# Optimization experiments

Hardware: AMD Instinct MI355X
Metric: run time of the kernel (lower is better)

The kernel has to match this reference:

```python
import jax, jax.numpy as jnp
import numpy as np

N_NODES = 100000
N_EDGES = 1600000
IN_CH, HID_CH, OUT_CH = 256, 128, 64


def setup_inputs() -> dict:
    key = jax.random.key(0)
    k_x, k_e, k1, k2, kb1, kb2 = jax.random.split(key, 6)
    x = jax.random.normal(k_x, (N_NODES, IN_CH), dtype=jnp.float32)
    edge_index = jax.random.randint(k_e, (2, N_EDGES), 0, N_NODES, dtype=jnp.int64)
    # Glorot-style init for GCN linear weights
    W1 = jax.random.normal(k1, (IN_CH, HID_CH), dtype=jnp.float32) * (1.0 / np.sqrt(IN_CH))
    b1 = jnp.zeros((HID_CH,), dtype=jnp.float32)
    W2 = jax.random.normal(k2, (HID_CH, OUT_CH), dtype=jnp.float32) * (1.0 / np.sqrt(HID_CH))
    b2 = jnp.zeros((OUT_CH,), dtype=jnp.float32)
    return {"x": x, "edge_index": edge_index, "W1": W1, "b1": b1, "W2": W2, "b2": b2}


def _gcn_norm(edge_index, n_nodes):
    # add self loops, compute D^{-1/2} (A+I) D^{-1/2} edge weights (PyG gcn_norm)
    loop = jnp.arange(n_nodes, dtype=edge_index.dtype)
    src = jnp.concatenate([edge_index[0], loop])
    dst = jnp.concatenate([edge_index[1], loop])
    deg = jax.ops.segment_sum(jnp.ones_like(src, dtype=jnp.float32), dst, num_segments=n_nodes)
    dinv = jnp.where(deg > 0, jax.lax.rsqrt(jnp.maximum(deg, 1.0)), 0.0)
    norm = dinv[src] * dinv[dst]  # [E + N]
    return src, dst, norm


def _gcn_conv(x, W, b, src, dst, norm, n_nodes):
    h = x @ W                         # linear first (PyG GCNConv)
    msg = norm[:, None] * h[src]      # gather + normalize  [E+N, out]
    agg = jax.ops.segment_sum(msg, dst, num_segments=n_nodes)
    return agg + b


def reference(x, edge_index, W1, b1, W2, b2):
    n = x.shape[0]
    src, dst, norm = _gcn_norm(edge_index, n)
    h = jax.nn.relu(_gcn_conv(x, W1, b1, src, dst, norm, n))
    # dropout is identity in eval mode
    z = _gcn_conv(h, W2, b2, src, dst, norm, n)
    # inner-product decoder on the provided edges, with sigmoid
    e_src, e_dst = edge_index[0], edge_index[1]
    logits = jnp.sum(z[e_src] * z[e_dst], axis=-1)
    return jax.nn.sigmoid(logits)
```

## Files before the change

kernel.cpp:

```cpp
#include <hip/hip_runtime.h>
#include <math.h>

#define N_NODES 100000
#define N_EDGES 1600000
#define IN_CH 256
#define HID_CH 128
#define OUT_CH 64
#define NTILES ((N_NODES + 63) / 64)
#define NB 1024
#define NPART 256
#define EPB (N_EDGES / NPART)
#define NB_USED ((N_NODES + 127) / 128)

typedef short s16x8 __attribute__((ext_vector_type(8)));
typedef unsigned short u16x8 __attribute__((ext_vector_type(8)));
typedef float f32x4 __attribute__((ext_vector_type(4)));

__device__ __forceinline__ float bf2f(unsigned short u) {
    union { unsigned int i; float f; } v;
    v.i = ((unsigned int)u) << 16;
    return v.f;
}
__device__ __forceinline__ unsigned short f2bf(float f) {
    union { float f; unsigned int i; } v;
    v.f = f;
    unsigned int u = v.i;
    return (unsigned short)((u + 0x7FFFu + ((u >> 16) & 1u)) >> 16);
}


__global__ __launch_bounds__(256) void k_hist(const int* __restrict__ dst,
                                              int* __restrict__ ghist) {
    __shared__ int h[NB];
    int b = blockIdx.x, t = threadIdx.x;
    for (int k = t; k < NB; k += 256) h[k] = 0;
    __syncthreads();
    int e0 = b * EPB;
    for (int e = e0 + t; e < e0 + EPB; e += 256)
        atomicAdd(&h[dst[e] >> 7], 1);
    __syncthreads();
    for (int k = t; k < NB; k += 256) ghist[k * NPART + b] = h[k];
}

__global__ __launch_bounds__(256) void k_scan_cols(const int* __restrict__ ghist,
                                                   int* __restrict__ goff,
                                                   int* __restrict__ btot) {
    __shared__ int tmp[NPART];
    int k = blockIdx.x, t = threadIdx.x;
    int v = ghist[k * NPART + t];
    tmp[t] = v;
    __syncthreads();
    for (int off = 1; off < NPART; off <<= 1) {
        int u = (t >= off) ? tmp[t - off] : 0;
        __syncthreads();
        tmp[t] += u;
        __syncthreads();
    }
    goff[k * NPART + t] = tmp[t] - v;
    if (t == NPART - 1) btot[k] = tmp[t];
}

__global__ __launch_bounds__(1024) void k_scan_base(const int* __restrict__ btot,
                                                    int* __restrict__ bbase) {
    __shared__ int tmp[NB];
    int t = threadIdx.x;
    int v = btot[t];
    tmp[t] = v;
    __syncthreads();
    for (int off = 1; off < NB; off <<= 1) {
        int u = (t >= off) ? tmp[t - off] : 0;
        __syncthreads();
        tmp[t] += u;
        __syncthreads();
    }
    bbase[t] = tmp[t] - v;
    if (t == NB - 1) bbase[NB] = tmp[t];
}

__global__ __launch_bounds__(256) void k_partition(const int* __restrict__ src,
                                                   const int* __restrict__ dst,
                                                   const int* __restrict__ goff,
                                                   const int* __restrict__ bbase,
                                                   int2* __restrict__ bsorted) {
    __shared__ int cur[NB];
    int b = blockIdx.x, t = threadIdx.x;
    for (int k = t; k < NB; k += 256) cur[k] = bbase[k] + goff[k * NPART + b];
    __syncthreads();
    int e0 = b * EPB;
    for (int e = e0 + t; e < e0 + EPB; e += 256) {
        int s = src[e], d = dst[e];
        int pos = atomicAdd(&cur[d >> 7], 1);
        bsorted[pos] = make_int2(s, d);
    }
}

__global__ __launch_bounds__(256) void k_bucket_csr(const int2* __restrict__ bsorted,
                                                    const int* __restrict__ bbase,
                                                    int* __restrict__ rowoff,
                                                    float* __restrict__ dinv,
                                                    int* __restrict__ csr_src) {
    __shared__ int cnt[128];
    __shared__ int tmp[256];
    __shared__ int cur[128];
    int b = blockIdx.x, t = threadIdx.x;
    int ebeg = bbase[b], eend = bbase[b + 1];
    if (t < 128) cnt[t] = 0;
    __syncthreads();
    for (int e = ebeg + t; e < eend; e += 256)
        atomicAdd(&cnt[bsorted[e].y & 127], 1);
    __syncthreads();
    int v = (t < 128) ? cnt[t] : 0;
    tmp[t] = v;
    __syncthreads();
    for (int off = 1; off < 256; off <<= 1) {
        int u = (t >= off) ? tmp[t - off] : 0;
        __syncthreads();
        tmp[t] += u;
        __syncthreads();
    }
    if (t < 128) {
        int base = ebeg + tmp[t] - v;
        cur[t] = base;
        int node = b * 128 + t;
        if (node < N_NODES) {
            rowoff[node] = base;
            dinv[node] = rsqrtf((float)v + 1.0f);
        }
    }
    __syncthreads();
    for (int e = ebeg + t; e < eend; e += 256) {
        int2 ed = bsorted[e];
        int pos = atomicAdd(&cur[ed.y & 127], 1);
        csr_src[pos] = ed.x;
    }
}

__global__ __launch_bounds__(256) void k_cast(const float* __restrict__ x,
                                              unsigned short* __restrict__ xb) {
    const int total = N_NODES * IN_CH / 8;
    int stride = gridDim.x * 256;
    for (int i = blockIdx.x * 256 + threadIdx.x; i < total; i += stride) {
        f32x4 a = *reinterpret_cast<const f32x4*>(x + (size_t)i * 8);
        f32x4 b = *reinterpret_cast<const f32x4*>(x + (size_t)i * 8 + 4);
        u16x8 o;
        o[0] = f2bf(a[0]); o[1] = f2bf(a[1]); o[2] = f2bf(a[2]); o[3] = f2bf(a[3]);
        o[4] = f2bf(b[0]); o[5] = f2bf(b[1]); o[6] = f2bf(b[2]); o[7] = f2bf(b[3]);
        *reinterpret_cast<u16x8*>(xb + (size_t)i * 8) = o;
    }
}

__global__ void k_wt1(const float* __restrict__ W1, unsigned short* __restrict__ Wf1) {
    int u = blockIdx.x * 256 + threadIdx.x;
    int f = u >> 6, lane = u & 63;
    int kk = f >> 3, nt = f & 7;
    int l15 = lane & 15, lhi = lane >> 4;
    int n = nt * 16 + l15;
    int kbase = kk * 32 + lhi * 8;
    #pragma unroll
    for (int j = 0; j < 8; ++j)
        Wf1[(size_t)u * 8 + j] = f2bf(W1[(size_t)(kbase + j) * HID_CH + n]);
}

__global__ void k_wt2(const float* __restrict__ W2, unsigned short* __restrict__ Wf2) {
    int u = blockIdx.x * 256 + threadIdx.x;
    int f = u >> 6, lane = u & 63;
    int kk = f >> 2, nt = f & 3;
    int l15 = lane & 15, lhi = lane >> 4;
    int n = nt * 16 + l15;
    int kbase = kk * 32 + lhi * 8;
    #pragma unroll
    for (int j = 0; j < 8; ++j)
        Wf2[(size_t)u * 8 + j] = f2bf(W2[(size_t)(kbase + j) * OUT_CH + n]);
}

__global__ __launch_bounds__(256, 4) void k_gemm1(const unsigned short* __restrict__ xb,
                                                  const unsigned short* __restrict__ Wf1,
                                                  const float* __restrict__ dinv,
                                                  unsigned short* __restrict__ hs1) {
    int tid = threadIdx.x;
    int w = tid >> 6;
    int lane = tid & 63;
    int l15 = lane & 15;
    int lhi = lane >> 4;
    int m0 = blockIdx.x * 64;

    int arow = m0 + w * 16 + l15;
    int arowc = (arow < N_NODES) ? arow : (N_NODES - 1);
    const s16x8* ap = reinterpret_cast<const s16x8*>(xb + (size_t)arowc * IN_CH) + lhi;

    s16x8 af[8];
    #pragma unroll
    for (int kk = 0; kk < 8; ++kk) af[kk] = ap[kk * 4];

    const s16x8* wp = reinterpret_cast<const s16x8*>(Wf1) + lane;

    f32x4 acc[8] = {};
    #pragma unroll
    for (int kk = 0; kk < 8; ++kk) {
        #pragma unroll
        for (int nt = 0; nt < 8; ++nt) {
            s16x8 bf = wp[(kk * 8 + nt) * 64];
            acc[nt] = __builtin_amdgcn_mfma_f32_16x16x32_bf16(af[kk], bf, acc[nt], 0, 0, 0);
        }
    }

    float dv[4];
    int rb = m0 + w * 16 + lhi * 4;
    #pragma unroll
    for (int r = 0; r < 4; ++r) dv[r] = (rb + r < N_NODES) ? dinv[rb + r] : 0.0f;
    #pragma unroll
    for (int nt = 0; nt < 8; ++nt) {
        #pragma unroll
        for (int r = 0; r < 4; ++r) {
            int row = rb + r;
            if (row < N_NODES)
                hs1[(size_t)row * HID_CH + nt * 16 + l15] = f2bf(dv[r] * acc[nt][r]);
        }
    }
}

__global__ __launch_bounds__(256, 4) void k_gemm2(const unsigned short* __restrict__ h1r,
                                                  const unsigned short* __restrict__ Wf2,
                                                  const float* __restrict__ dinv,
                                                  unsigned short* __restrict__ hs2) {
    int tid = threadIdx.x;
    int w = tid >> 6;
    int lane = tid & 63;
    int l15 = lane & 15;
    int lhi = lane >> 4;
    int m0 = blockIdx.x * 64;

    int arow = m0 + w * 16 + l15;
    int arowc = (arow < N_NODES) ? arow : (N_NODES - 1);
    const s16x8* ap = reinterpret_cast<const s16x8*>(h1r + (size_t)arowc * HID_CH) + lhi;

    s16x8 af[4];
    #pragma unroll
    for (int kk = 0; kk < 4; ++kk) af[kk] = ap[kk * 4];

    const s16x8* wp = reinterpret_cast<const s16x8*>(Wf2) + lane;

    f32x4 acc[4] = {};
    #pragma unroll
    for (int kk = 0; kk < 4; ++kk) {
        #pragma unroll
        for (int nt = 0; nt < 4; ++nt) {
            s16x8 bf = wp[(kk * 4 + nt) * 64];
            acc[nt] = __builtin_amdgcn_mfma_f32_16x16x32_bf16(af[kk], bf, acc[nt], 0, 0, 0);
        }
    }

    float dv[4];
    int rb = m0 + w * 16 + lhi * 4;
    #pragma unroll
    for (int r = 0; r < 4; ++r) dv[r] = (rb + r < N_NODES) ? dinv[rb + r] : 0.0f;
    #pragma unroll
    for (int nt = 0; nt < 4; ++nt) {
        #pragma unroll
        for (int r = 0; r < 4; ++r) {
            int row = rb + r;
            if (row < N_NODES)
                hs2[(size_t)row * OUT_CH + nt * 16 + l15] = f2bf(dv[r] * acc[nt][r]);
        }
    }
}

template <int C, bool RELU>
__global__ __launch_bounds__(256) void k_gather_agg(const int* __restrict__ rowoff,
                                                    const int* __restrict__ csr_src,
                                                    const unsigned short* __restrict__ hs,
                                                    const float* __restrict__ dinv,
                                                    const float* __restrict__ b,
                                                    unsigned short* __restrict__ outp) {
    constexpr int TPN = C / 8;
    constexpr int NPB = 256 / TPN;
    int t = threadIdx.x;
    int node = blockIdx.x * NPB + t / TPN;
    int q = t % TPN;
    if (node >= N_NODES) return;

    int beg = rowoff[node];
    int end = (node + 1 < N_NODES) ? rowoff[node + 1] : N_EDGES;

    float acc[8];
    {
        u16x8 sv = *reinterpret_cast<const u16x8*>(&hs[(size_t)node * C + q * 8]);
        #pragma unroll
        for (int j = 0; j < 8; ++j) acc[j] = bf2f(sv[j]);
    }

    int i = beg;
    for (; i + 1 < end; i += 2) {
        int s0 = csr_src[i];
        int s1 = csr_src[i + 1];
        u16x8 v0 = *reinterpret_cast<const u16x8*>(&hs[(size_t)s0 * C + q * 8]);
        u16x8 v1 = *reinterpret_cast<const u16x8*>(&hs[(size_t)s1 * C + q * 8]);
        #pragma unroll
        for (int j = 0; j < 8; ++j) acc[j] += bf2f(v0[j]) + bf2f(v1[j]);
    }
    if (i < end) {
        int s0 = csr_src[i];
        u16x8 v0 = *reinterpret_cast<const u16x8*>(&hs[(size_t)s0 * C + q * 8]);
        #pragma unroll
        for (int j = 0; j < 8; ++j) acc[j] += bf2f(v0[j]);
    }

    float w = dinv[node];
    float4 b0 = reinterpret_cast<const float4*>(b)[q * 2];
    float4 b1 = reinterpret_cast<const float4*>(b)[q * 2 + 1];
    float bb[8] = {b0.x, b0.y, b0.z, b0.w, b1.x, b1.y, b1.z, b1.w};
    u16x8 o;
    #pragma unroll
    for (int j = 0; j < 8; ++j) {
        float v = w * acc[j] + bb[j];
        if (RELU) v = fmaxf(v, 0.0f);
        o[j] = f2bf(v);
    }
    *reinterpret_cast<u16x8*>(&outp[(size_t)node * C + q * 8]) = o;
}


__global__ __launch_bounds__(256) void k_decode(const int* __restrict__ esrc,
                                                const int* __restrict__ edst,
                                                const unsigned short* __restrict__ z,
                                                float* __restrict__ out) {
    int tid = threadIdx.x;
    int e = blockIdx.x * 32 + tid / 8;
    int q = tid % 8;
    if (e >= N_EDGES) return;
    int s = esrc[e], d = edst[e];
    u16x8 a = *reinterpret_cast<const u16x8*>(&z[(size_t)s * OUT_CH + q * 8]);
    u16x8 b = *reinterpret_cast<const u16x8*>(&z[(size_t)d * OUT_CH + q * 8]);
    float dot = 0.0f;
    #pragma unroll
    for (int j = 0; j < 8; ++j) dot += bf2f(a[j]) * bf2f(b[j]);
    dot += __shfl_xor(dot, 1);
    dot += __shfl_xor(dot, 2);
    dot += __shfl_xor(dot, 4);
    if (q == 0) out[e] = 1.0f / (1.0f + expf(-dot));
}


extern "C" void kernel_launch(void* const* d_in, const int* in_sizes, int n_in,
                              void* d_out, int out_size, void* d_ws, size_t ws_size,
                              hipStream_t stream) {
    const float* x  = (const float*)d_in[0];
    const int*   ei = (const int*)d_in[1];
    const float* W1 = (const float*)d_in[2];
    const float* b1 = (const float*)d_in[3];
    const float* W2 = (const float*)d_in[4];
    const float* b2 = (const float*)d_in[5];
    float* out = (float*)d_out;

    const int* src = ei;
    const int* dst = ei + N_EDGES;

    char* ws = (char*)d_ws;
    int*   ghist   = (int*)(ws + 0x000000);
    int*   goff    = (int*)(ws + 0x100000);
    int*   btot    = (int*)(ws + 0x200000);
    int*   bbase   = (int*)(ws + 0x202000);
    int*   rowoff  = (int*)(ws + 0x210000);
    float* dinv    = (float*)(ws + 0x290000);
    unsigned short* Wf1 = (unsigned short*)(ws + 0x310000);
    unsigned short* Wf2 = (unsigned short*)(ws + 0x320000);
    int*   csr_src = (int*)(ws + 0x400000);
    int2*  bsorted = (int2*)(ws + 0xB00000);
    unsigned short* xb  = (unsigned short*)(ws + 0xB00000);
    unsigned short* hs1 = (unsigned short*)(ws + 0x3C00000);
    unsigned short* h1r = (unsigned short*)(ws + 0xB00000);
    unsigned short* hs2 = (unsigned short*)(ws + 0x3C00000);
    unsigned short* z   = (unsigned short*)(ws + 0x2800000);

    k_hist<<<NPART, 256, 0, stream>>>(dst, ghist);
    k_scan_cols<<<NB, 256, 0, stream>>>(ghist, goff, btot);
    k_scan_base<<<1, NB, 0, stream>>>(btot, bbase);
    k_partition<<<NPART, 256, 0, stream>>>(src, dst, goff, bbase, bsorted);
    k_bucket_csr<<<NB_USED, 256, 0, stream>>>(bsorted, bbase, rowoff, dinv, csr_src);

    k_cast<<<2048, 256, 0, stream>>>(x, xb);
    k_wt1<<<16, 256, 0, stream>>>(W1, Wf1);
    k_wt2<<<4, 256, 0, stream>>>(W2, Wf2);

    k_gemm1<<<NTILES, 256, 0, stream>>>(xb, Wf1, dinv, hs1);
    k_gather_agg<HID_CH, true><<<(N_NODES * 16 + 255) / 256, 256, 0, stream>>>(
        rowoff, csr_src, hs1, dinv, b1, h1r);

    k_gemm2<<<NTILES, 256, 0, stream>>>(h1r, Wf2, dinv, hs2);
    k_gather_agg<OUT_CH, false><<<(N_NODES * 8 + 255) / 256, 256, 0, stream>>>(
        rowoff, csr_src, hs2, dinv, b2, z);

    k_decode<<<N_EDGES / 32, 256, 0, stream>>>(src, dst, z, out);
}
```

Before: 264.3 us.

## Slice GEMM outputs into 16-column planes and gather per plane with LDS-staged indices

The GEMM epilogues now write their outputs as column-sliced planes of 16 channels (32 bytes per node), so each aggregation pass touches a small plane that fits better in cache. A 2D grid processes one plane per blockIdx.y for 128 nodes, staging the CSR source indices for those nodes in shared memory and unrolling the neighbor loop by four. In exchange, the index list is loaded once per plane and each gathered row is only 32 bytes. The GEMM stores also become more scattered.

```diff
diff --git a/kernel.cpp b/kernel.cpp
--- a/kernel.cpp
+++ b/kernel.cpp
@@ -11,6 +11,7 @@
 #define NPART 256
 #define EPB (N_EDGES / NPART)
 #define NB_USED ((N_NODES + 127) / 128)
+#define LCAP 4096
 
 typedef short s16x8 __attribute__((ext_vector_type(8)));
 typedef unsigned short u16x8 __attribute__((ext_vector_type(8)));
@@ -176,7 +177,7 @@
 __global__ __launch_bounds__(256, 4) void k_gemm1(const unsigned short* __restrict__ xb,
                                                   const unsigned short* __restrict__ Wf1,
                                                   const float* __restrict__ dinv,
-                                                  unsigned short* __restrict__ hs1) {
+                                                  unsigned short* __restrict__ hs1s) {
     int tid = threadIdx.x;
     int w = tid >> 6;
     int lane = tid & 63;
@@ -214,7 +215,7 @@
         for (int r = 0; r < 4; ++r) {
             int row = rb + r;
             if (row < N_NODES)
-                hs1[(size_t)row * HID_CH + nt * 16 + l15] = f2bf(dv[r] * acc[nt][r]);
+                hs1s[((size_t)nt * N_NODES + row) * 16 + l15] = f2bf(dv[r] * acc[nt][r]);
         }
     }
 }
@@ -222,7 +223,7 @@
 __global__ __launch_bounds__(256, 4) void k_gemm2(const unsigned short* __restrict__ h1r,
                                                   const unsigned short* __restrict__ Wf2,
                                                   const float* __restrict__ dinv,
-                                                  unsigned short* __restrict__ hs2) {
+                                                  unsigned short* __restrict__ hs2s) {
     int tid = threadIdx.x;
     int w = tid >> 6;
     int lane = tid & 63;
@@ -260,54 +261,73 @@
         for (int r = 0; r < 4; ++r) {
             int row = rb + r;
             if (row < N_NODES)
-                hs2[(size_t)row * OUT_CH + nt * 16 + l15] = f2bf(dv[r] * acc[nt][r]);
+                hs2s[((size_t)nt * N_NODES + row) * 16 + l15] = f2bf(dv[r] * acc[nt][r]);
         }
     }
 }
 
 template <int C, bool RELU>
-__global__ __launch_bounds__(256) void k_gather_agg(const int* __restrict__ rowoff,
-                                                    const int* __restrict__ csr_src,
-                                                    const unsigned short* __restrict__ hs,
-                                                    const float* __restrict__ dinv,
-                                                    const float* __restrict__ b,
-                                                    unsigned short* __restrict__ outp) {
-    constexpr int TPN = C / 8;
-    constexpr int NPB = 256 / TPN;
-    int t = threadIdx.x;
-    int node = blockIdx.x * NPB + t / TPN;
-    int q = t % TPN;
+__global__ __launch_bounds__(256) void k_gather_sl(const int* __restrict__ rowoff,
+                                                   const int* __restrict__ csr_src,
+                                                   const unsigned short* __restrict__ hsS,
+                                                   const float* __restrict__ dinv,
+                                                   const float* __restrict__ b,
+                                                   unsigned short* __restrict__ outp) {
+    __shared__ int lidx[LCAP];
+    int bx = blockIdx.x, p = blockIdx.y, t = threadIdx.x;
+    int n0 = bx * 128;
+    int ebeg = rowoff[n0];
+    int eend = (n0 + 128 < N_NODES) ? rowoff[n0 + 128] : N_EDGES;
+    int cnt = eend - ebeg;
+
+    for (int i = t; i < cnt && i < LCAP; i += 256) lidx[i] = csr_src[ebeg + i];
+    __syncthreads();
+
+    int node = n0 + (t >> 1);
+    int q = t & 1;
     if (node >= N_NODES) return;
 
-    int beg = rowoff[node];
-    int end = (node + 1 < N_NODES) ? rowoff[node + 1] : N_EDGES;
+    const unsigned short* P = hsS + (size_t)p * N_NODES * 16;
+    int lbeg = rowoff[node] - ebeg;
+    int lend = ((node + 1 < N_NODES) ? rowoff[node + 1] : N_EDGES) - ebeg;
 
     float acc[8];
     {
-        u16x8 sv = *reinterpret_cast<const u16x8*>(&hs[(size_t)node * C + q * 8]);
+        u16x8 sv = *reinterpret_cast<const u16x8*>(P + ((size_t)node << 4) + (q << 3));
         #pragma unroll
         for (int j = 0; j < 8; ++j) acc[j] = bf2f(sv[j]);
     }
 
-    int i = beg;
-    for (; i + 1 < end; i += 2) {
-        int s0 = csr_src[i];
-        int s1 = csr_src[i + 1];
-        u16x8 v0 = *reinterpret_cast<const u16x8*>(&hs[(size_t)s0 * C + q * 8]);
-        u16x8 v1 = *reinterpret_cast<const u16x8*>(&hs[(size_t)s1 * C + q * 8]);
-        #pragma unroll
-        for (int j = 0; j < 8; ++j) acc[j] += bf2f(v0[j]) + bf2f(v1[j]);
-    }
-    if (i < end) {
-        int s0 = csr_src[i];
-        u16x8 v0 = *reinterpret_cast<const u16x8*>(&hs[(size_t)s0 * C + q * 8]);
-        #pragma unroll
-        for (int j = 0; j < 8; ++j) acc[j] += bf2f(v0[j]);
+    if (cnt <= LCAP) {
+        int i = lbeg;
+        for (; i + 3 < lend; i += 4) {
+            int s0 = lidx[i], s1 = lidx[i + 1], s2 = lidx[i + 2], s3 = lidx[i + 3];
+            u16x8 v0 = *reinterpret_cast<const u16x8*>(P + ((size_t)s0 << 4) + (q << 3));
+            u16x8 v1 = *reinterpret_cast<const u16x8*>(P + ((size_t)s1 << 4) + (q << 3));
+            u16x8 v2 = *reinterpret_cast<const u16x8*>(P + ((size_t)s2 << 4) + (q << 3));
+            u16x8 v3 = *reinterpret_cast<const u16x8*>(P + ((size_t)s3 << 4) + (q << 3));
+            #pragma unroll
+            for (int j = 0; j < 8; ++j)
+                acc[j] += (bf2f(v0[j]) + bf2f(v1[j])) + (bf2f(v2[j]) + bf2f(v3[j]));
+        }
+        for (; i < lend; ++i) {
+            int s0 = lidx[i];
+            u16x8 v0 = *reinterpret_cast<const u16x8*>(P + ((size_t)s0 << 4) + (q << 3));
+            #pragma unroll
+            for (int j = 0; j < 8; ++j) acc[j] += bf2f(v0[j]);
+        }
+    } else {
+        for (int i = lbeg; i < lend; ++i) {
+            int s0 = csr_src[ebeg + i];
+            u16x8 v0 = *reinterpret_cast<const u16x8*>(P + ((size_t)s0 << 4) + (q << 3));
+            #pragma unroll
+            for (int j = 0; j < 8; ++j) acc[j] += bf2f(v0[j]);
+        }
     }
 
     float w = dinv[node];
-    float4 b0 = reinterpret_cast<const float4*>(b)[q * 2];
-    float4 b1 = reinterpret_cast<const float4*>(b)[q * 2 + 1];
+    float4 b0 = *reinterpret_cast<const float4*>(&b[p * 16 + q * 8]);
+    float4 b1 = *reinterpret_cast<const float4*>(&b[p * 16 + q * 8 + 4]);
     float bb[8] = {b0.x, b0.y, b0.z, b0.w, b1.x, b1.y, b1.z, b1.w};
     u16x8 o;
     #pragma unroll
@@ -316,7 +336,7 @@
         if (RELU) v = fmaxf(v, 0.0f);
         o[j] = f2bf(v);
     }
-    *reinterpret_cast<u16x8*>(&outp[(size_t)node * C + q * 8]) = o;
+    *reinterpret_cast<u16x8*>(outp + (size_t)node * C + p * 16 + (q << 3)) = o;
 }
 
 
@@ -366,11 +386,11 @@
     unsigned short* Wf2 = (unsigned short*)(ws + 0x320000);
     int*   csr_src = (int*)(ws + 0x400000);
     int2*  bsorted = (int2*)(ws + 0xB00000);
-    unsigned short* xb  = (unsigned short*)(ws + 0xB00000);
-    unsigned short* hs1 = (unsigned short*)(ws + 0x3C00000);
-    unsigned short* h1r = (unsigned short*)(ws + 0xB00000);
-    unsigned short* hs2 = (unsigned short*)(ws + 0x3C00000);
-    unsigned short* z   = (unsigned short*)(ws + 0x2800000);
+    unsigned short* xb   = (unsigned short*)(ws + 0xB00000);
+    unsigned short* hs1s = (unsigned short*)(ws + 0x3C00000);
+    unsigned short* h1r  = (unsigned short*)(ws + 0xB00000);
+    unsigned short* hs2s = (unsigned short*)(ws + 0x3C00000);
+    unsigned short* z    = (unsigned short*)(ws + 0x2800000);
 
     k_hist<<<NPART, 256, 0, stream>>>(dst, ghist);
     k_scan_cols<<<NB, 256, 0, stream>>>(ghist, goff, btot);
@@ -382,13 +402,13 @@
     k_wt1<<<16, 256, 0, stream>>>(W1, Wf1);
     k_wt2<<<4, 256, 0, stream>>>(W2, Wf2);
 
-    k_gemm1<<<NTILES, 256, 0, stream>>>(xb, Wf1, dinv, hs1);
-    k_gather_agg<HID_CH, true><<<(N_NODES * 16 + 255) / 256, 256, 0, stream>>>(
-        rowoff, csr_src, hs1, dinv, b1, h1r);
-
-    k_gemm2<<<NTILES, 256, 0, stream>>>(h1r, Wf2, dinv, hs2);
-    k_gather_agg<OUT_CH, false><<<(N_NODES * 8 + 255) / 256, 256, 0, stream>>>(
-        rowoff, csr_src, hs2, dinv, b2, z);
+    k_gemm1<<<NTILES, 256, 0, stream>>>(xb, Wf1, dinv, hs1s);
+    k_gather_sl<HID_CH, true><<<dim3(NB_USED, HID_CH / 16), 256, 0, stream>>>(
+        rowoff, csr_src, hs1s, dinv, b1, h1r);
+
+    k_gemm2<<<NTILES, 256, 0, stream>>>(h1r, Wf2, dinv, hs2s);
+    k_gather_sl<OUT_CH, false><<<dim3(NB_USED, OUT_CH / 16), 256, 0, stream>>>(
+        rowoff, csr_src, hs2s, dinv, b2, z);
 
     k_decode<<<N_EDGES / 32, 256, 0, stream>>>(src, dst, z, out);
 }
```

After: 301.0 us. +13.9%, slower.

## Fuse layer-1 aggregation with layer-2 GEMM via shared-memory tile

Applied to the files above, without the earlier changes.

Layer-1 neighbor aggregation (bias plus ReLU) now runs in the same kernel as the second linear layer. Each block aggregates 64 nodes into a swizzled LDS tile and feeds it straight to MFMA, so the h1 round trip through global memory and one launch go away. The generic gather kernel also unrolls its edge loop by four for more memory-level parallelism. In exchange, each thread now handles 32 channels per node instead of 8, which means fewer threads per node, more registers per thread, and possibly lower occupancy or worse latency hiding in the gather.

```diff
diff --git a/kernel.cpp b/kernel.cpp
--- a/kernel.cpp
+++ b/kernel.cpp
@@ -219,39 +219,104 @@
     }
 }
 
-__global__ __launch_bounds__(256, 4) void k_gemm2(const unsigned short* __restrict__ h1r,
-                                                  const unsigned short* __restrict__ Wf2,
-                                                  const float* __restrict__ dinv,
-                                                  unsigned short* __restrict__ hs2) {
-    int tid = threadIdx.x;
-    int w = tid >> 6;
-    int lane = tid & 63;
+__global__ __launch_bounds__(256) void k_agg_gemm2(const int* __restrict__ rowoff,
+                                                   const int* __restrict__ csr_src,
+                                                   const unsigned short* __restrict__ hs1,
+                                                   const float* __restrict__ dinv,
+                                                   const float* __restrict__ b1,
+                                                   const unsigned short* __restrict__ Wf2,
+                                                   unsigned short* __restrict__ hs2) {
+    __shared__ unsigned short tile[64 * 128];
+    int t = threadIdx.x;
+    int n0 = blockIdx.x * 64;
+    int nl = t >> 2;
+    int q = t & 3;
+    int node = n0 + nl;
+    bool valid = node < N_NODES;
+    int nodec = valid ? node : (N_NODES - 1);
+
+    int beg = 0, end = 0;
+    if (valid) {
+        beg = rowoff[node];
+        end = (node + 1 < N_NODES) ? rowoff[node + 1] : N_EDGES;
+    }
+
+    const unsigned short* base = hs1 + q * 32;
+
+    float acc[4][8];
+    #pragma unroll
+    for (int j = 0; j < 4; ++j) {
+        u16x8 v = *reinterpret_cast<const u16x8*>(base + (size_t)nodec * HID_CH + j * 8);
+        #pragma unroll
+        for (int c = 0; c < 8; ++c) acc[j][c] = bf2f(v[c]);
+    }
+
+    int i = beg;
+    for (; i + 1 < end; i += 2) {
+        int s0 = csr_src[i], s1 = csr_src[i + 1];
+        u16x8 v0[4], v1[4];
+        #pragma unroll
+        for (int j = 0; j < 4; ++j)
+            v0[j] = *reinterpret_cast<const u16x8*>(base + (size_t)s0 * HID_CH + j * 8);
+        #pragma unroll
+        for (int j = 0; j < 4; ++j)
+            v1[j] = *reinterpret_cast<const u16x8*>(base + (size_t)s1 * HID_CH + j * 8);
+        #pragma unroll
+        for (int j = 0; j < 4; ++j)
+            #pragma unroll
+            for (int c = 0; c < 8; ++c) acc[j][c] += bf2f(v0[j][c]) + bf2f(v1[j][c]);
+    }
+    if (i < end) {
+        int s0 = csr_src[i];
+        #pragma unroll
+        for (int j = 0; j < 4; ++j) {
+            u16x8 v0 = *reinterpret_cast<const u16x8*>(base + (size_t)s0 * HID_CH + j * 8);
+            #pragma unroll
+            for (int c = 0; c < 8; ++c) acc[j][c] += bf2f(v0[c]);
+        }
+    }
+
+    float w = valid ? dinv[node] : 0.0f;
+    #pragma unroll
+    for (int j = 0; j < 4; ++j) {
+        float4 ba = *reinterpret_cast<const float4*>(b1 + q * 32 + j * 8);
+        float4 bb = *reinterpret_cast<const float4*>(b1 + q * 32 + j * 8 + 4);
+        float bv[8] = {ba.x, ba.y, ba.z, ba.w, bb.x, bb.y, bb.z, bb.w};
+        u16x8 o;
+        #pragma unroll
+        for (int c = 0; c < 8; ++c)
+            o[c] = f2bf(fmaxf(w * acc[j][c] + bv[c], 0.0f));
+        int u = (q * 4 + j) ^ (nl & 15);
+        *reinterpret_cast<u16x8*>(&tile[nl * 128 + u * 8]) = o;
+    }
+    __syncthreads();
+
+    int w4 = t >> 6;
+    int lane = t & 63;
     int l15 = lane & 15;
     int lhi = lane >> 4;
-    int m0 = blockIdx.x * 64;
-
-    int arow = m0 + w * 16 + l15;
-    int arowc = (arow < N_NODES) ? arow : (N_NODES - 1);
-    const s16x8* ap = reinterpret_cast<const s16x8*>(h1r + (size_t)arowc * HID_CH) + lhi;
+    int R = w4 * 16 + l15;
 
     s16x8 af[4];
     #pragma unroll
-    for (int kk = 0; kk < 4; ++kk) af[kk] = ap[kk * 4];
+    for (int kk = 0; kk < 4; ++kk) {
+        int cu = (kk * 4 + lhi) ^ (R & 15);
+        af[kk] = *reinterpret_cast<const s16x8*>(&tile[R * 128 + cu * 8]);
+    }
 
     const s16x8* wp = reinterpret_cast<const s16x8*>(Wf2) + lane;
-
-    f32x4 acc[4] = {};
+    f32x4 acc2[4] = {};
     #pragma unroll
     for (int kk = 0; kk < 4; ++kk) {
         #pragma unroll
         for (int nt = 0; nt < 4; ++nt) {
             s16x8 bf = wp[(kk * 4 + nt) * 64];
-            acc[nt] = __builtin_amdgcn_mfma_f32_16x16x32_bf16(af[kk], bf, acc[nt], 0, 0, 0);
+            acc2[nt] = __builtin_amdgcn_mfma_f32_16x16x32_bf16(af[kk], bf, acc2[nt], 0, 0, 0);
         }
     }
 
     float dv[4];
-    int rb = m0 + w * 16 + lhi * 4;
+    int rb = n0 + w4 * 16 + lhi * 4;
     #pragma unroll
     for (int r = 0; r < 4; ++r) dv[r] = (rb + r < N_NODES) ? dinv[rb + r] : 0.0f;
     #pragma unroll
@@ -260,7 +325,7 @@
         for (int r = 0; r < 4; ++r) {
             int row = rb + r;
             if (row < N_NODES)
-                hs2[(size_t)row * OUT_CH + nt * 16 + l15] = f2bf(dv[r] * acc[nt][r]);
+                hs2[(size_t)row * OUT_CH + nt * 16 + l15] = f2bf(dv[r] * acc2[nt][r]);
         }
     }
 }
@@ -290,15 +355,17 @@
     }
 
     int i = beg;
-    for (; i + 1 < end; i += 2) {
-        int s0 = csr_src[i];
-        int s1 = csr_src[i + 1];
+    for (; i + 3 < end; i += 4) {
+        int s0 = csr_src[i], s1 = csr_src[i + 1], s2 = csr_src[i + 2], s3 = csr_src[i + 3];
         u16x8 v0 = *reinterpret_cast<const u16x8*>(&hs[(size_t)s0 * C + q * 8]);
         u16x8 v1 = *reinterpret_cast<const u16x8*>(&hs[(size_t)s1 * C + q * 8]);
-        #pragma unroll
-        for (int j = 0; j < 8; ++j) acc[j] += bf2f(v0[j]) + bf2f(v1[j]);
-    }
-    if (i < end) {
+        u16x8 v2 = *reinterpret_cast<const u16x8*>(&hs[(size_t)s2 * C + q * 8]);
+        u16x8 v3 = *reinterpret_cast<const u16x8*>(&hs[(size_t)s3 * C + q * 8]);
+        #pragma unroll
+        for (int j = 0; j < 8; ++j)
+            acc[j] += (bf2f(v0[j]) + bf2f(v1[j])) + (bf2f(v2[j]) + bf2f(v3[j]));
+    }
+    for (; i < end; ++i) {
         int s0 = csr_src[i];
         u16x8 v0 = *reinterpret_cast<const u16x8*>(&hs[(size_t)s0 * C + q * 8]);
         #pragma unroll
@@ -368,8 +435,7 @@
     int2*  bsorted = (int2*)(ws + 0xB00000);
     unsigned short* xb  = (unsigned short*)(ws + 0xB00000);
     unsigned short* hs1 = (unsigned short*)(ws + 0x3C00000);
-    unsigned short* h1r = (unsigned short*)(ws + 0xB00000);
-    unsigned short* hs2 = (unsigned short*)(ws + 0x3C00000);
+    unsigned short* hs2 = (unsigned short*)(ws + 0xB00000);
     unsigned short* z   = (unsigned short*)(ws + 0x2800000);
 
     k_hist<<<NPART, 256, 0, stream>>>(dst, ghist);
@@ -383,10 +449,9 @@
     k_wt2<<<4, 256, 0, stream>>>(W2, Wf2);
 
     k_gemm1<<<NTILES, 256, 0, stream>>>(xb, Wf1, dinv, hs1);
-    k_gather_agg<HID_CH, true><<<(N_NODES * 16 + 255) / 256, 256, 0, stream>>>(
-        rowoff, csr_src, hs1, dinv, b1, h1r);
-
-    k_gemm2<<<NTILES, 256, 0, stream>>>(h1r, Wf2, dinv, hs2);
+
+    k_agg_gemm2<<<NTILES, 256, 0, stream>>>(rowoff, csr_src, hs1, dinv, b1, Wf2, hs2);
+
     k_gather_agg<OUT_CH, false><<<(N_NODES * 8 + 255) / 256, 256, 0, stream>>>(
         rowoff, csr_src, hs2, dinv, b2, z);
 
```

After: 262.6 us. No clear change (-0.6%).

## Split layer-1 features into 16-channel planes for cache-local gather

Applied to the files above, without the earlier changes.

GEMM1 now writes its output as 8 column planes of 16 bf16 channels each, 3.2 MB per plane. A new gather kernel aggregates one plane per block, with blocks interleaved across planes, so each gather pass works on a small working set that can stay in cache. GEMM2 reads its A operand from this planar layout. Both gather loops are also unrolled from 2 to 4 neighbours to give more memory-level parallelism. The cost is eight times more passes over the CSR indices and smaller 32-byte gathers per edge.

```diff
diff --git a/kernel.cpp b/kernel.cpp
--- a/kernel.cpp
+++ b/kernel.cpp
@@ -176,7 +176,7 @@
 __global__ __launch_bounds__(256, 4) void k_gemm1(const unsigned short* __restrict__ xb,
                                                   const unsigned short* __restrict__ Wf1,
                                                   const float* __restrict__ dinv,
-                                                  unsigned short* __restrict__ hs1) {
+                                                  unsigned short* __restrict__ hs1s) {
     int tid = threadIdx.x;
     int w = tid >> 6;
     int lane = tid & 63;
@@ -214,12 +214,67 @@
         for (int r = 0; r < 4; ++r) {
             int row = rb + r;
             if (row < N_NODES)
-                hs1[(size_t)row * HID_CH + nt * 16 + l15] = f2bf(dv[r] * acc[nt][r]);
+                hs1s[((size_t)nt * N_NODES + row) * 16 + l15] = f2bf(dv[r] * acc[nt][r]);
         }
     }
 }
 
-__global__ __launch_bounds__(256, 4) void k_gemm2(const unsigned short* __restrict__ h1r,
+__global__ __launch_bounds__(256) void k_gather_sx1(const int* __restrict__ rowoff,
+                                                    const int* __restrict__ csr_src,
+                                                    const unsigned short* __restrict__ hs1s,
+                                                    const float* __restrict__ dinv,
+                                                    const float* __restrict__ b1,
+                                                    unsigned short* __restrict__ h1rs) {
+    int b = blockIdx.x;
+    int p = b & 7;
+    int idx = b >> 3;
+    int t = threadIdx.x;
+    int node = idx * 128 + (t >> 1);
+    int q = t & 1;
+    if (node >= N_NODES) return;
+
+    const unsigned short* P = hs1s + (size_t)p * N_NODES * 16 + q * 8;
+
+    int beg = rowoff[node];
+    int end = (node + 1 < N_NODES) ? rowoff[node + 1] : N_EDGES;
+
+    float acc[8];
+    {
+        u16x8 sv = *reinterpret_cast<const u16x8*>(P + (size_t)node * 16);
+        #pragma unroll
+        for (int c = 0; c < 8; ++c) acc[c] = bf2f(sv[c]);
+    }
+
+    int i = beg;
+    for (; i + 3 < end; i += 4) {
+        int s0 = csr_src[i], s1 = csr_src[i + 1], s2 = csr_src[i + 2], s3 = csr_src[i + 3];
+        u16x8 v0 = *reinterpret_cast<const u16x8*>(P + (size_t)s0 * 16);
+        u16x8 v1 = *reinterpret_cast<const u16x8*>(P + (size_t)s1 * 16);
+        u16x8 v2 = *reinterpret_cast<const u16x8*>(P + (size_t)s2 * 16);
+        u16x8 v3 = *reinterpret_cast<const u16x8*>(P + (size_t)s3 * 16);
+        #pragma unroll
+        for (int c = 0; c < 8; ++c)
+            acc[c] += (bf2f(v0[c]) + bf2f(v1[c])) + (bf2f(v2[c]) + bf2f(v3[c]));
+    }
+    for (; i < end; ++i) {
+        int s0 = csr_src[i];
+        u16x8 v0 = *reinterpret_cast<const u16x8*>(P + (size_t)s0 * 16);
+        #pragma unroll
+        for (int c = 0; c < 8; ++c) acc[c] += bf2f(v0[c]);
+    }
+
+    float w = dinv[node];
+    float4 ba = *reinterpret_cast<const float4*>(b1 + p * 16 + q * 8);
+    float4 bb = *reinterpret_cast<const float4*>(b1 + p * 16 + q * 8 + 4);
+    float bv[8] = {ba.x, ba.y, ba.z, ba.w, bb.x, bb.y, bb.z, bb.w};
+    u16x8 o;
+    #pragma unroll
+    for (int c = 0; c < 8; ++c)
+        o[c] = f2bf(fmaxf(w * acc[c] + bv[c], 0.0f));
+    *reinterpret_cast<u16x8*>(h1rs + ((size_t)p * N_NODES + node) * 16 + q * 8) = o;
+}
+
+__global__ __launch_bounds__(256, 4) void k_gemm2(const unsigned short* __restrict__ h1rs,
                                                   const unsigned short* __restrict__ Wf2,
                                                   const float* __restrict__ dinv,
                                                   unsigned short* __restrict__ hs2) {
@@ -232,14 +287,16 @@
 
     int arow = m0 + w * 16 + l15;
     int arowc = (arow < N_NODES) ? arow : (N_NODES - 1);
-    const s16x8* ap = reinterpret_cast<const s16x8*>(h1r + (size_t)arowc * HID_CH) + lhi;
 
     s16x8 af[4];
     #pragma unroll
-    for (int kk = 0; kk < 4; ++kk) af[kk] = ap[kk * 4];
+    for (int kk = 0; kk < 4; ++kk) {
+        int plane = 2 * kk + (lhi >> 1);
+        af[kk] = *reinterpret_cast<const s16x8*>(
+            h1rs + ((size_t)plane * N_NODES + arowc) * 16 + (lhi & 1) * 8);
+    }
 
     const s16x8* wp = reinterpret_cast<const s16x8*>(Wf2) + lane;
-
     f32x4 acc[4] = {};
     #pragma unroll
     for (int kk = 0; kk < 4; ++kk) {
@@ -290,15 +347,17 @@
     }
 
     int i = beg;
-    for (; i + 1 < end; i += 2) {
-        int s0 = csr_src[i];
-        int s1 = csr_src[i + 1];
+    for (; i + 3 < end; i += 4) {
+        int s0 = csr_src[i], s1 = csr_src[i + 1], s2 = csr_src[i + 2], s3 = csr_src[i + 3];
         u16x8 v0 = *reinterpret_cast<const u16x8*>(&hs[(size_t)s0 * C + q * 8]);
         u16x8 v1 = *reinterpret_cast<const u16x8*>(&hs[(size_t)s1 * C + q * 8]);
-        #pragma unroll
-        for (int j = 0; j < 8; ++j) acc[j] += bf2f(v0[j]) + bf2f(v1[j]);
-    }
-    if (i < end) {
+        u16x8 v2 = *reinterpret_cast<const u16x8*>(&hs[(size_t)s2 * C + q * 8]);
+        u16x8 v3 = *reinterpret_cast<const u16x8*>(&hs[(size_t)s3 * C + q * 8]);
+        #pragma unroll
+        for (int j = 0; j < 8; ++j)
+            acc[j] += (bf2f(v0[j]) + bf2f(v1[j])) + (bf2f(v2[j]) + bf2f(v3[j]));
+    }
+    for (; i < end; ++i) {
         int s0 = csr_src[i];
         u16x8 v0 = *reinterpret_cast<const u16x8*>(&hs[(size_t)s0 * C + q * 8]);
         #pragma unroll
@@ -366,11 +425,11 @@
     unsigned short* Wf2 = (unsigned short*)(ws + 0x320000);
     int*   csr_src = (int*)(ws + 0x400000);
     int2*  bsorted = (int2*)(ws + 0xB00000);
-    unsigned short* xb  = (unsigned short*)(ws + 0xB00000);
-    unsigned short* hs1 = (unsigned short*)(ws + 0x3C00000);
-    unsigned short* h1r = (unsigned short*)(ws + 0xB00000);
-    unsigned short* hs2 = (unsigned short*)(ws + 0x3C00000);
-    unsigned short* z   = (unsigned short*)(ws + 0x2800000);
+    unsigned short* xb   = (unsigned short*)(ws + 0xB00000);
+    unsigned short* hs1s = (unsigned short*)(ws + 0x3C00000);
+    unsigned short* h1rs = (unsigned short*)(ws + 0xB00000);
+    unsigned short* hs2  = (unsigned short*)(ws + 0x2800000);
+    unsigned short* z    = (unsigned short*)(ws + 0x3C00000);
 
     k_hist<<<NPART, 256, 0, stream>>>(dst, ghist);
     k_scan_cols<<<NB, 256, 0, stream>>>(ghist, goff, btot);
@@ -382,11 +441,10 @@
     k_wt1<<<16, 256, 0, stream>>>(W1, Wf1);
     k_wt2<<<4, 256, 0, stream>>>(W2, Wf2);
 
-    k_gemm1<<<NTILES, 256, 0, stream>>>(xb, Wf1, dinv, hs1);
-    k_gather_agg<HID_CH, true><<<(N_NODES * 16 + 255) / 256, 256, 0, stream>>>(
-        rowoff, csr_src, hs1, dinv, b1, h1r);
-
-    k_gemm2<<<NTILES, 256, 0, stream>>>(h1r, Wf2, dinv, hs2);
+    k_gemm1<<<NTILES, 256, 0, stream>>>(xb, Wf1, dinv, hs1s);
+    k_gather_sx1<<<8 * NB_USED, 256, 0, stream>>>(rowoff, csr_src, hs1s, dinv, b1, h1rs);
+
+    k_gemm2<<<NTILES, 256, 0, stream>>>(h1rs, Wf2, dinv, hs2);
     k_gather_agg<OUT_CH, false><<<(N_NODES * 8 + 255) / 256, 256, 0, stream>>>(
         rowoff, csr_src, hs2, dinv, b2, z);
 
```

Measured after the change: 284.6 us. +7.7%, slower.
